# Optimization experiments

Hardware: AMD Instinct MI355X
Metric: run time of the kernel (lower is better)

Reference implementation:

```python
import jax, jax.numpy as jnp
import numpy as np

TAU = 0.1
EPS_NORM = 1e-12
EPS_DENOM = 1e-8


def _l2norm(x):
    # F.normalize(x, dim=1): x / max(||x||, eps)
    n = jnp.linalg.norm(x, axis=1, keepdims=True)
    return x / jnp.maximum(n, EPS_NORM)


def setup_inputs() -> dict:
    key = jax.random.key(0)
    ks = jax.random.split(key, 8)
    D, N_POS, N_HARD, N_MIX = 512, 8192, 65536, 64
    return {
        "anchor": jax.random.normal(ks[0], (1, D), dtype=jnp.float32),
        "positives": jax.random.normal(ks[1], (N_POS, D), dtype=jnp.float32),
        "hard_negatives": jax.random.normal(ks[2], (N_HARD, D), dtype=jnp.float32),
        "mix_idx": jax.random.randint(ks[3], (N_MIX,), 0, N_HARD, dtype=jnp.int32),
        "idx_a": jax.random.randint(ks[4], (N_MIX,), 0, N_HARD, dtype=jnp.int32),
        "idx_b": jax.random.randint(ks[5], (N_MIX,), 0, N_HARD, dtype=jnp.int32),
        "alpha_raw": jax.random.uniform(ks[6], (N_MIX, 1), dtype=jnp.float32),
        "beta_raw": jax.random.uniform(ks[7], (N_MIX, 1), dtype=jnp.float32),
    }


def reference(anchor, positives, hard_negatives, mix_idx, idx_a, idx_b, alpha_raw, beta_raw):
    a = _l2norm(anchor)            # [1, D]
    p = _l2norm(positives)         # [N_pos, D]
    h = _l2norm(hard_negatives)    # [N_hard, D]

    # MoCHi synthesis: anchor-mixed hardest negatives
    alpha = alpha_raw * 0.4 + 0.1                      # [N_mix, 1] in [0.1, 0.5)
    hardest = _l2norm((1.0 - alpha) * h[mix_idx] + alpha * a)
    # negative-negative mixes
    beta = beta_raw * 0.4 + 0.3                        # [N_mix, 1] in [0.3, 0.7)
    harder = _l2norm(beta * h[idx_a] + (1.0 - beta) * h[idx_b])

    all_negs = jnp.concatenate([h, hardest, harder], axis=0)  # [N_hard + 128, D]

    av = a[0]                                  # [D]
    pos_logits = (p @ av) / TAU                # [N_pos]
    neg_logits = (all_negs @ av) / TAU         # [N_neg]

    neg_sum_exp = jnp.sum(jnp.exp(neg_logits))
    pos_val = jnp.exp(pos_logits)
    # original: mean_i of -log(exp(l_i) / (exp(l_i) + neg_sum_exp + 1e-8))
    loss = jnp.mean(-jnp.log(pos_val / (pos_val + neg_sum_exp + EPS_DENOM)))
    return loss
```

## Files before the change

kernel.cpp:

```cpp
#include <hip/hip_runtime.h>
#include <hip/hip_bf16.h>
#include <math.h>

#define TAU_F       0.1f
#define EPS_NORM_F  1e-12f
#define EPS_DENOM_F 1e-8f

__device__ __forceinline__ float dot4(float4 a, float4 b) {
    return a.x * b.x + a.y * b.y + a.z * b.z + a.w * b.w;
}

__global__ void __launch_bounds__(256) rows_kernel(
        const float* __restrict__ anchor,
        const float* __restrict__ pos,
        const float* __restrict__ hn,
        float* __restrict__ cos_h,
        float* __restrict__ cos_p,
        double* __restrict__ S_acc,
        int n_hard, int n_pos) {
    const int lane = threadIdx.x & 63;
    const int wib  = threadIdx.x >> 6;
    const int wpb  = blockDim.x >> 6;
    const int wid  = blockIdx.x * wpb + wib;
    const int nw   = gridDim.x * wpb;

    const float4* a4 = (const float4*)anchor;
    const float4 a0 = a4[lane];
    const float4 a1 = a4[lane + 64];

    float na2 = dot4(a0, a0) + dot4(a1, a1);
    #pragma unroll
    for (int o = 32; o > 0; o >>= 1) na2 += __shfl_xor(na2, o, 64);
    const float na = fmaxf(sqrtf(na2), EPS_NORM_F);

    const int total = n_hard + n_pos;
    float local_exp = 0.0f;

    for (int r = wid; r < total; r += nw) {
        const bool is_h = (r < n_hard);
        const float4* row = is_h ? (const float4*)hn + (size_t)r * 128
                                 : (const float4*)pos + (size_t)(r - n_hard) * 128;
        const float4 v0 = row[lane];
        const float4 v1 = row[lane + 64];
        float s  = dot4(v0, a0) + dot4(v1, a1);
        float n2 = dot4(v0, v0) + dot4(v1, v1);
        #pragma unroll
        for (int o = 32; o > 0; o >>= 1) {
            s  += __shfl_xor(s,  o, 64);
            n2 += __shfl_xor(n2, o, 64);
        }
        const float nrm  = fmaxf(sqrtf(n2), EPS_NORM_F);
        const float cosv = s / (nrm * na);
        if (is_h) {
            if (lane == 0) cos_h[r] = cosv;
            local_exp += __expf(cosv / TAU_F) * 0.0f + expf(cosv / TAU_F);
        } else {
            if (lane == 0) cos_p[r - n_hard] = cosv;
        }
    }

    __shared__ float sred[16];
    if (lane == 0) sred[wib] = local_exp;
    __syncthreads();
    if (threadIdx.x == 0) {
        float t = 0.0f;
        for (int i = 0; i < wpb; ++i) t += sred[i];
        atomicAdd(S_acc, (double)t);
    }
}

__global__ void __launch_bounds__(256) mix_kernel(
        const float* __restrict__ hn,
        const float* __restrict__ cos_h,
        const int* __restrict__ mix_idx,
        const int* __restrict__ idx_a,
        const int* __restrict__ idx_b,
        const float* __restrict__ alpha_raw,
        const float* __restrict__ beta_raw,
        double* __restrict__ S_acc,
        int n_mix) {
    const int lane = threadIdx.x & 63;
    const int wib  = threadIdx.x >> 6;
    const int wpb  = blockDim.x >> 6;
    const int j    = blockIdx.x * wpb + wib;

    float e = 0.0f;

    if (j < n_mix) {
        if (lane == 0) {
            const float c  = cos_h[mix_idx[j]];
            const float al = alpha_raw[j] * 0.4f + 0.1f;
            const float num  = (1.0f - al) * c + al;
            const float den2 = (1.0f - al) * (1.0f - al) + al * al
                             + 2.0f * al * (1.0f - al) * c;
            const float cosm = num / fmaxf(sqrtf(den2), EPS_NORM_F);
            e = expf(cosm / TAU_F);
        }
    } else if (j < 2 * n_mix) {
        const int k  = j - n_mix;
        const int ra = idx_a[k];
        const int rb = idx_b[k];
        const float4* A = (const float4*)hn + (size_t)ra * 128;
        const float4* B = (const float4*)hn + (size_t)rb * 128;
        const float4 x0 = A[lane], x1 = A[lane + 64];
        const float4 y0 = B[lane], y1 = B[lane + 64];
        float d   = dot4(x0, y0) + dot4(x1, y1);
        float na2 = dot4(x0, x0) + dot4(x1, x1);
        float nb2 = dot4(y0, y0) + dot4(y1, y1);
        #pragma unroll
        for (int o = 32; o > 0; o >>= 1) {
            d   += __shfl_xor(d,   o, 64);
            na2 += __shfl_xor(na2, o, 64);
            nb2 += __shfl_xor(nb2, o, 64);
        }
        if (lane == 0) {
            const float na  = fmaxf(sqrtf(na2), EPS_NORM_F);
            const float nb  = fmaxf(sqrtf(nb2), EPS_NORM_F);
            const float dab = d / (na * nb);
            const float be  = beta_raw[k] * 0.4f + 0.3f;
            const float ca  = cos_h[ra];
            const float cb  = cos_h[rb];
            const float num  = be * ca + (1.0f - be) * cb;
            const float den2 = be * be + (1.0f - be) * (1.0f - be)
                             + 2.0f * be * (1.0f - be) * dab;
            const float cosm = num / fmaxf(sqrtf(den2), EPS_NORM_F);
            e = expf(cosm / TAU_F);
        }
    }

    __shared__ float sred[16];
    if (lane == 0) sred[wib] = e;
    __syncthreads();
    if (threadIdx.x == 0) {
        float t = 0.0f;
        for (int i = 0; i < wpb; ++i) t += sred[i];
        atomicAdd(S_acc, (double)t);
    }
}

__global__ void __launch_bounds__(256) loss_kernel(
        const float* __restrict__ cos_p,
        const double* __restrict__ S_acc,
        float* __restrict__ out,
        int n_pos) {
    __shared__ double sred[256];
    const float S = (float)S_acc[0];
    double acc = 0.0;
    for (int i = threadIdx.x; i < n_pos; i += blockDim.x) {
        const float l  = cos_p[i] / TAU_F;
        const float pv = expf(l);
        acc += (double)(-logf(pv / (pv + S + EPS_DENOM_F)));
    }
    sred[threadIdx.x] = acc;
    __syncthreads();
    for (int s = blockDim.x >> 1; s > 0; s >>= 1) {
        if (threadIdx.x < (unsigned)s) sred[threadIdx.x] += sred[threadIdx.x + s];
        __syncthreads();
    }
    if (threadIdx.x == 0) out[0] = (float)(sred[0] / (double)n_pos);
}

extern "C" void kernel_launch(void* const* d_in, const int* in_sizes, int n_in,
                              void* d_out, int out_size, void* d_ws, size_t ws_size,
                              hipStream_t stream) {
    const float* anchor    = (const float*)d_in[0];
    const float* positives = (const float*)d_in[1];
    const float* hardnegs  = (const float*)d_in[2];
    const int*   mix_idx   = (const int*)d_in[3];
    const int*   idx_a     = (const int*)d_in[4];
    const int*   idx_b     = (const int*)d_in[5];
    const float* alpha_raw = (const float*)d_in[6];
    const float* beta_raw  = (const float*)d_in[7];

    const int D      = in_sizes[0];
    const int n_pos  = in_sizes[1] / D;
    const int n_hard = in_sizes[2] / D;
    const int n_mix  = in_sizes[3];

    char*   ws    = (char*)d_ws;
    double* S_acc = (double*)ws;
    float*  cos_h = (float*)(ws + 16);
    float*  cos_p = cos_h + n_hard;

    hipMemsetAsync(S_acc, 0, sizeof(double), stream);

    rows_kernel<<<2048, 256, 0, stream>>>(anchor, positives, hardnegs,
                                          cos_h, cos_p, S_acc, n_hard, n_pos);

    const int mix_waves  = 2 * n_mix;
    const int mix_blocks = (mix_waves + 3) / 4;
    mix_kernel<<<mix_blocks, 256, 0, stream>>>(hardnegs, cos_h, mix_idx, idx_a,
                                               idx_b, alpha_raw, beta_raw,
                                               S_acc, n_mix);

    loss_kernel<<<1, 256, 0, stream>>>(cos_p, S_acc, (float*)d_out, n_pos);
}
```

Baseline: 244.8 us.

## Fuse rows, mix and loss kernels into one launch with last-block reduction

Merges the three kernels into a single kernel. The mix-negative terms are recomputed from the original rows by the first waves, so the cos_h buffer and its writes go away. The final loss is computed by the last block to finish, detected with an atomic counter, and the double-precision atomic accumulator is replaced by a per-block sums array. This removes two kernel launches and the inter-kernel gaps, but the whole loss tail now runs serially in one block at the end.

```diff
diff --git a/kernel.cpp b/kernel.cpp
--- a/kernel.cpp
+++ b/kernel.cpp
@@ -1,5 +1,4 @@
 #include <hip/hip_runtime.h>
-#include <hip/hip_bf16.h>
 #include <math.h>
 
 #define TAU_F       0.1f
@@ -10,14 +9,20 @@
     return a.x * b.x + a.y * b.y + a.z * b.z + a.w * b.w;
 }
 
-__global__ void __launch_bounds__(256) rows_kernel(
+__global__ void __launch_bounds__(256) fused_kernel(
         const float* __restrict__ anchor,
         const float* __restrict__ pos,
         const float* __restrict__ hn,
-        float* __restrict__ cos_h,
+        const int* __restrict__ mix_idx,
+        const int* __restrict__ idx_a,
+        const int* __restrict__ idx_b,
+        const float* __restrict__ alpha_raw,
+        const float* __restrict__ beta_raw,
+        float* __restrict__ out,
+        double* __restrict__ block_sums,
         float* __restrict__ cos_p,
-        double* __restrict__ S_acc,
-        int n_hard, int n_pos) {
+        unsigned* __restrict__ ctr,
+        int n_hard, int n_pos, int n_mix) {
     const int lane = threadIdx.x & 63;
     const int wib  = threadIdx.x >> 6;
     const int wpb  = blockDim.x >> 6;
@@ -27,15 +32,14 @@
     const float4* a4 = (const float4*)anchor;
     const float4 a0 = a4[lane];
     const float4 a1 = a4[lane + 64];
-
     float na2 = dot4(a0, a0) + dot4(a1, a1);
     #pragma unroll
     for (int o = 32; o > 0; o >>= 1) na2 += __shfl_xor(na2, o, 64);
     const float na = fmaxf(sqrtf(na2), EPS_NORM_F);
 
-    const int total = n_hard + n_pos;
     float local_exp = 0.0f;
 
+    const int total = n_hard + n_pos;
     for (int r = wid; r < total; r += nw) {
         const bool is_h = (r < n_hard);
         const float4* row = is_h ? (const float4*)hn + (size_t)r * 128
@@ -52,112 +56,106 @@
         const float nrm  = fmaxf(sqrtf(n2), EPS_NORM_F);
         const float cosv = s / (nrm * na);
         if (is_h) {
-            if (lane == 0) cos_h[r] = cosv;
-            local_exp += __expf(cosv / TAU_F) * 0.0f + expf(cosv / TAU_F);
-        } else {
-            if (lane == 0) cos_p[r - n_hard] = cosv;
+            local_exp += expf(cosv / TAU_F);
+        } else if (lane == 0) {
+            cos_p[r - n_hard] = cosv;
         }
     }
 
+    if (wid < n_mix) {
+        const int j = wid;
+        const float4* R = (const float4*)hn + (size_t)mix_idx[j] * 128;
+        const float4 v0 = R[lane], v1 = R[lane + 64];
+        float s  = dot4(v0, a0) + dot4(v1, a1);
+        float n2 = dot4(v0, v0) + dot4(v1, v1);
+        #pragma unroll
+        for (int o = 32; o > 0; o >>= 1) {
+            s  += __shfl_xor(s,  o, 64);
+            n2 += __shfl_xor(n2, o, 64);
+        }
+        const float nrm = fmaxf(sqrtf(n2), EPS_NORM_F);
+        const float c   = s / (nrm * na);
+        const float al  = alpha_raw[j] * 0.4f + 0.1f;
+        const float num  = (1.0f - al) * c + al;
+        const float den2 = (1.0f - al) * (1.0f - al) + al * al
+                         + 2.0f * al * (1.0f - al) * c;
+        const float cosm = num / fmaxf(sqrtf(den2), EPS_NORM_F);
+        local_exp += expf(cosm / TAU_F);
+    } else if (wid < 2 * n_mix) {
+        const int k  = wid - n_mix;
+        const float4* A = (const float4*)hn + (size_t)idx_a[k] * 128;
+        const float4* B = (const float4*)hn + (size_t)idx_b[k] * 128;
+        const float4 x0 = A[lane], x1 = A[lane + 64];
+        const float4 y0 = B[lane], y1 = B[lane + 64];
+        float sa  = dot4(x0, a0) + dot4(x1, a1);
+        float sb  = dot4(y0, a0) + dot4(y1, a1);
+        float d   = dot4(x0, y0) + dot4(x1, y1);
+        float nA2 = dot4(x0, x0) + dot4(x1, x1);
+        float nB2 = dot4(y0, y0) + dot4(y1, y1);
+        #pragma unroll
+        for (int o = 32; o > 0; o >>= 1) {
+            sa  += __shfl_xor(sa,  o, 64);
+            sb  += __shfl_xor(sb,  o, 64);
+            d   += __shfl_xor(d,   o, 64);
+            nA2 += __shfl_xor(nA2, o, 64);
+            nB2 += __shfl_xor(nB2, o, 64);
+        }
+        const float nA  = fmaxf(sqrtf(nA2), EPS_NORM_F);
+        const float nB  = fmaxf(sqrtf(nB2), EPS_NORM_F);
+        const float ca  = sa / (nA * na);
+        const float cb  = sb / (nB * na);
+        const float dab = d  / (nA * nB);
+        const float be  = beta_raw[k] * 0.4f + 0.3f;
+        const float num  = be * ca + (1.0f - be) * cb;
+        const float den2 = be * be + (1.0f - be) * (1.0f - be)
+                         + 2.0f * be * (1.0f - be) * dab;
+        const float cosm = num / fmaxf(sqrtf(den2), EPS_NORM_F);
+        local_exp += expf(cosm / TAU_F);
+    }
+
     __shared__ float sred[16];
+    __shared__ int   is_last;
     if (lane == 0) sred[wib] = local_exp;
     __syncthreads();
     if (threadIdx.x == 0) {
         float t = 0.0f;
         for (int i = 0; i < wpb; ++i) t += sred[i];
-        atomicAdd(S_acc, (double)t);
+        block_sums[blockIdx.x] = (double)t;
+        __threadfence();
+        const unsigned old = __hip_atomic_fetch_add(
+            ctr, 1u, __ATOMIC_ACQ_REL, __HIP_MEMORY_SCOPE_AGENT);
+        is_last = (old == (unsigned)gridDim.x - 1u) ? 1 : 0;
     }
-}
+    __syncthreads();
+    if (!is_last) return;
 
-__global__ void __launch_bounds__(256) mix_kernel(
-        const float* __restrict__ hn,
-        const float* __restrict__ cos_h,
-        const int* __restrict__ mix_idx,
-        const int* __restrict__ idx_a,
-        const int* __restrict__ idx_b,
-        const float* __restrict__ alpha_raw,
-        const float* __restrict__ beta_raw,
-        double* __restrict__ S_acc,
-        int n_mix) {
-    const int lane = threadIdx.x & 63;
-    const int wib  = threadIdx.x >> 6;
-    const int wpb  = blockDim.x >> 6;
-    const int j    = blockIdx.x * wpb + wib;
+    __threadfence();
 
-    float e = 0.0f;
-
-    if (j < n_mix) {
-        if (lane == 0) {
-            const float c  = cos_h[mix_idx[j]];
-            const float al = alpha_raw[j] * 0.4f + 0.1f;
-            const float num  = (1.0f - al) * c + al;
-            const float den2 = (1.0f - al) * (1.0f - al) + al * al
-                             + 2.0f * al * (1.0f - al) * c;
-            const float cosm = num / fmaxf(sqrtf(den2), EPS_NORM_F);
-            e = expf(cosm / TAU_F);
-        }
-    } else if (j < 2 * n_mix) {
-        const int k  = j - n_mix;
-        const int ra = idx_a[k];
-        const int rb = idx_b[k];
-        const float4* A = (const float4*)hn + (size_t)ra * 128;
-        const float4* B = (const float4*)hn + (size_t)rb * 128;
-        const float4 x0 = A[lane], x1 = A[lane + 64];
-        const float4 y0 = B[lane], y1 = B[lane + 64];
-        float d   = dot4(x0, y0) + dot4(x1, y1);
-        float na2 = dot4(x0, x0) + dot4(x1, x1);
-        float nb2 = dot4(y0, y0) + dot4(y1, y1);
-        #pragma unroll
-        for (int o = 32; o > 0; o >>= 1) {
-            d   += __shfl_xor(d,   o, 64);
-            na2 += __shfl_xor(na2, o, 64);
-            nb2 += __shfl_xor(nb2, o, 64);
-        }
-        if (lane == 0) {
-            const float na  = fmaxf(sqrtf(na2), EPS_NORM_F);
-            const float nb  = fmaxf(sqrtf(nb2), EPS_NORM_F);
-            const float dab = d / (na * nb);
-            const float be  = beta_raw[k] * 0.4f + 0.3f;
-            const float ca  = cos_h[ra];
-            const float cb  = cos_h[rb];
-            const float num  = be * ca + (1.0f - be) * cb;
-            const float den2 = be * be + (1.0f - be) * (1.0f - be)
-                             + 2.0f * be * (1.0f - be) * dab;
-            const float cosm = num / fmaxf(sqrtf(den2), EPS_NORM_F);
-            e = expf(cosm / TAU_F);
-        }
-    }
-
-    __shared__ float sred[16];
-    if (lane == 0) sred[wib] = e;
+    __shared__ double dred[256];
+    double acc = 0.0;
+    for (int i = threadIdx.x; i < (int)gridDim.x; i += blockDim.x)
+        acc += block_sums[i];
+    dred[threadIdx.x] = acc;
     __syncthreads();
-    if (threadIdx.x == 0) {
-        float t = 0.0f;
-        for (int i = 0; i < wpb; ++i) t += sred[i];
-        atomicAdd(S_acc, (double)t);
-    }
-}
-
-__global__ void __launch_bounds__(256) loss_kernel(
-        const float* __restrict__ cos_p,
-        const double* __restrict__ S_acc,
-        float* __restrict__ out,
-        int n_pos) {
-    __shared__ double sred[256];
-    const float S = (float)S_acc[0];
-    double acc = 0.0;
-    for (int i = threadIdx.x; i < n_pos; i += blockDim.x) {
-        const float l  = cos_p[i] / TAU_F;
-        const float pv = expf(l);
-        acc += (double)(-logf(pv / (pv + S + EPS_DENOM_F)));
-    }
-    sred[threadIdx.x] = acc;
-    __syncthreads();
-    for (int s = blockDim.x >> 1; s > 0; s >>= 1) {
-        if (threadIdx.x < (unsigned)s) sred[threadIdx.x] += sred[threadIdx.x + s];
+    for (int sft = 128; sft > 0; sft >>= 1) {
+        if (threadIdx.x < sft) dred[threadIdx.x] += dred[threadIdx.x + sft];
         __syncthreads();
     }
-    if (threadIdx.x == 0) out[0] = (float)(sred[0] / (double)n_pos);
+    const float S = (float)dred[0];
+    __syncthreads();
+
+    double lacc = 0.0;
+    for (int i = threadIdx.x; i < n_pos; i += blockDim.x) {
+        const float pv = expf(cos_p[i] / TAU_F);
+        lacc += (double)(-logf(pv / (pv + S + EPS_DENOM_F)));
+    }
+    dred[threadIdx.x] = lacc;
+    __syncthreads();
+    for (int sft = 128; sft > 0; sft >>= 1) {
+        if (threadIdx.x < sft) dred[threadIdx.x] += dred[threadIdx.x + sft];
+        __syncthreads();
+    }
+    if (threadIdx.x == 0) out[0] = (float)(dred[0] / (double)n_pos);
 }
 
 extern "C" void kernel_launch(void* const* d_in, const int* in_sizes, int n_in,
@@ -177,21 +175,18 @@
     const int n_hard = in_sizes[2] / D;
     const int n_mix  = in_sizes[3];
 
-    char*   ws    = (char*)d_ws;
-    double* S_acc = (double*)ws;
-    float*  cos_h = (float*)(ws + 16);
-    float*  cos_p = cos_h + n_hard;
+    const int GRID = 2048;
 
-    hipMemsetAsync(S_acc, 0, sizeof(double), stream);
+    char*     ws         = (char*)d_ws;
+    unsigned* ctr        = (unsigned*)ws;
+    double*   block_sums = (double*)(ws + 1024);
+    float*    cos_p      = (float*)(ws + 1024 + (size_t)GRID * sizeof(double));
 
-    rows_kernel<<<2048, 256, 0, stream>>>(anchor, positives, hardnegs,
-                                          cos_h, cos_p, S_acc, n_hard, n_pos);
+    hipMemsetAsync(ctr, 0, sizeof(unsigned), stream);
 
-    const int mix_waves  = 2 * n_mix;
-    const int mix_blocks = (mix_waves + 3) / 4;
-    mix_kernel<<<mix_blocks, 256, 0, stream>>>(hardnegs, cos_h, mix_idx, idx_a,
-                                               idx_b, alpha_raw, beta_raw,
-                                               S_acc, n_mix);
-
-    loss_kernel<<<1, 256, 0, stream>>>(cos_p, S_acc, (float*)d_out, n_pos);
+    fused_kernel<<<GRID, 256, 0, stream>>>(anchor, positives, hardnegs,
+                                           mix_idx, idx_a, idx_b,
+                                           alpha_raw, beta_raw,
+                                           (float*)d_out, block_sums, cos_p, ctr,
+                                           n_hard, n_pos, n_mix);
 }
```

Measured after the change: 357.3 us. +45.9%, slower.
